# Kernel tuning notes

Measured on AMD Instinct MI355X. Metric: run time of the kernel, lower is better.

The kernel has to match this reference:

```python
import jax, jax.numpy as jnp
import numpy as np

N_OCC, N_SKILL, N_EDGE = 20000, 50000, 600000
D_IN, HID, OUT = 256, 128, 64


def _sage(x_src, x_dst, src, dst, Wl, bl, Wr, n_dst):
    """PyG SAGEConv((in,in),out): mean-aggregate neighbor msgs, lin_l + lin_r(x_dst)."""
    msg = x_src[src]                                        # [E, h] gather
    agg = jax.ops.segment_sum(msg, dst, num_segments=n_dst) # [n_dst, h]
    cnt = jax.ops.segment_sum(jnp.ones((src.shape[0],), x_src.dtype), dst,
                              num_segments=n_dst)
    mean = agg / jnp.maximum(cnt, 1.0)[:, None]
    return mean @ Wl + bl + x_dst @ Wr


def setup_inputs() -> dict:
    key = jax.random.key(0)
    ks = jax.random.split(key, 24)
    f32 = jnp.float32

    def lin(k, fi, fo):
        return jax.random.normal(k, (fi, fo), f32) / np.sqrt(fi)

    inp = {
        "x_occ": jax.random.normal(ks[0], (N_OCC, D_IN), f32),
        "x_skill": jax.random.normal(ks[1], (N_SKILL, D_IN), f32),
        "edge_occ": jax.random.randint(ks[2], (N_EDGE,), 0, N_OCC, jnp.int32),
        "edge_skill": jax.random.randint(ks[3], (N_EDGE,), 0, N_SKILL, jnp.int32),
        # input projections (nn.Linear with bias)
        "pW_occ": lin(ks[4], D_IN, HID), "pb_occ": jnp.zeros((HID,), f32),
        "pW_skill": lin(ks[5], D_IN, HID), "pb_skill": jnp.zeros((HID,), f32),
        # conv1: occ->skill and skill->occ SAGEConvs (lin_l has bias, lin_r none)
        "c1_os_Wl": lin(ks[6], HID, HID), "c1_os_bl": jnp.zeros((HID,), f32),
        "c1_os_Wr": lin(ks[7], HID, HID),
        "c1_so_Wl": lin(ks[8], HID, HID), "c1_so_bl": jnp.zeros((HID,), f32),
        "c1_so_Wr": lin(ks[9], HID, HID),
        # conv2
        "c2_os_Wl": lin(ks[10], HID, OUT), "c2_os_bl": jnp.zeros((OUT,), f32),
        "c2_os_Wr": lin(ks[11], HID, OUT),
        "c2_so_Wl": lin(ks[12], HID, OUT), "c2_so_bl": jnp.zeros((OUT,), f32),
        "c2_so_Wr": lin(ks[13], HID, OUT),
    }
    return inp


def reference(x_occ, x_skill, edge_occ, edge_skill,
              pW_occ, pb_occ, pW_skill, pb_skill,
              c1_os_Wl, c1_os_bl, c1_os_Wr, c1_so_Wl, c1_so_bl, c1_so_Wr,
              c2_os_Wl, c2_os_bl, c2_os_Wr, c2_so_Wl, c2_so_bl, c2_so_Wr):
    n_occ, n_skill = x_occ.shape[0], x_skill.shape[0]
    # input proj + relu
    h_occ = jax.nn.relu(x_occ @ pW_occ + pb_occ)
    h_skill = jax.nn.relu(x_skill @ pW_skill + pb_skill)
    # conv1 (HeteroConv aggr='sum'; each node type receives exactly one conv)
    s1 = _sage(h_occ, h_skill, edge_occ, edge_skill, c1_os_Wl, c1_os_bl, c1_os_Wr, n_skill)
    o1 = _sage(h_skill, h_occ, edge_skill, edge_occ, c1_so_Wl, c1_so_bl, c1_so_Wr, n_occ)
    o1, s1 = jax.nn.relu(o1), jax.nn.relu(s1)
    # conv2
    s2 = _sage(o1, s1, edge_occ, edge_skill, c2_os_Wl, c2_os_bl, c2_os_Wr, n_skill)
    o2 = _sage(s1, o1, edge_skill, edge_occ, c2_so_Wl, c2_so_bl, c2_so_Wr, n_occ)
    return o2, s2
```

## Files before the change

kernel.cpp:

```cpp
#include <hip/hip_runtime.h>

#define N_OCC   20000
#define N_SKILL 50000
#define N_EDGE  600000
#define D_IN    256
#define HID     128
#define OUT_F   64

typedef short bf16x8 __attribute__((ext_vector_type(8)));
typedef float f32x4  __attribute__((ext_vector_type(4)));

__device__ __forceinline__ float bf2f(unsigned short u){
  return __uint_as_float(((unsigned)u) << 16);
}
__device__ __forceinline__ unsigned f2bf_bits(float f){
  unsigned i = __float_as_uint(f);
  return (i + 0x7fffu + ((i >> 16) & 1u)) >> 16;
}
__device__ __forceinline__ unsigned f2bf_bits_u(unsigned i){
  return (i + 0x7fffu + ((i >> 16) & 1u)) >> 16;
}
__device__ __forceinline__ unsigned short f2bf(float f){ return (unsigned short)f2bf_bits(f); }

__device__ __forceinline__ void gload_lds16(const void* g, void* l){
  __builtin_amdgcn_global_load_lds(
      (const __attribute__((address_space(1))) unsigned int*)g,
      (__attribute__((address_space(3))) unsigned int*)l, 16, 0, 0);
}

__global__ void k_detect(const unsigned short* __restrict__ x, int* __restrict__ flag){
  int lane = threadIdx.x & 63;
  int cnt = 0;
  for (int i = lane; i < 1024; i += 64){
    unsigned e = ((unsigned)x[i] >> 7) & 0xFFu;
    if (e >= 0xE0u) cnt++;
  }
  #pragma unroll
  for (int s = 1; s < 64; s <<= 1) cnt += __shfl_xor(cnt, s, 64);
  if (lane == 0) *flag = (cnt >= 8) ? 1 : 0;
}

#define NT_CONV 18
struct ConvTable {
  const void*     src[NT_CONV];
  unsigned short* dst[NT_CONV];
  int             n[NT_CONV];
  int             isx[NT_CONV];
  int             blk_off[NT_CONV + 1];
};

__global__ void k_convert(ConvTable t, const int* __restrict__ flag){
  int isf32 = *flag;
  int b = blockIdx.x;
  int ti = 0;
  while (ti < NT_CONV - 1 && b >= t.blk_off[ti + 1]) ti++;
  if (!isf32 && t.isx[ti]) return;
  int lb = b - t.blk_off[ti];
  int i = (lb * 256 + (int)threadIdx.x) * 8;
  if (i >= t.n[ti]) return;
  unsigned short* dst = t.dst[ti];
  if (isf32){
    const float* s = (const float*)t.src[ti];
    uint4 lo = *(const uint4*)(s + i);
    uint4 hi = *(const uint4*)(s + i + 4);
    uint4 o;
    o.x = f2bf_bits_u(lo.x) | (f2bf_bits_u(lo.y) << 16);
    o.y = f2bf_bits_u(lo.z) | (f2bf_bits_u(lo.w) << 16);
    o.z = f2bf_bits_u(hi.x) | (f2bf_bits_u(hi.y) << 16);
    o.w = f2bf_bits_u(hi.z) | (f2bf_bits_u(hi.w) << 16);
    *(uint4*)(dst + i) = o;
  } else {
    *(uint4*)(dst + i) = *(const uint4*)((const unsigned short*)t.src[ti] + i);
  }
}

__global__ void k_transpose_all(
    const unsigned short* pWo, unsigned short* tWo,
    const unsigned short* pWs, unsigned short* tWs,
    const unsigned short* w2,  unsigned short* t2,
    const unsigned short* w3,  unsigned short* t3,
    const unsigned short* w4,  unsigned short* t4,
    const unsigned short* w5,  unsigned short* t5,
    const unsigned short* w6,  unsigned short* t6,
    const unsigned short* w7,  unsigned short* t7,
    const unsigned short* w8,  unsigned short* t8,
    const unsigned short* w9,  unsigned short* t9)
{
  int idx = blockIdx.x * blockDim.x + threadIdx.x;
  const unsigned short* in; unsigned short* out; int K, N, base;
  if      (idx <  32768){ in=pWo; out=tWo; K=256; N=128; base=0; }
  else if (idx <  65536){ in=pWs; out=tWs; K=256; N=128; base=32768; }
  else if (idx <  81920){ in=w2;  out=t2;  K=128; N=128; base=65536; }
  else if (idx <  98304){ in=w3;  out=t3;  K=128; N=128; base=81920; }
  else if (idx < 114688){ in=w4;  out=t4;  K=128; N=128; base=98304; }
  else if (idx < 131072){ in=w5;  out=t5;  K=128; N=128; base=114688; }
  else if (idx < 139264){ in=w6;  out=t6;  K=128; N=64;  base=131072; }
  else if (idx < 147456){ in=w7;  out=t7;  K=128; N=64;  base=139264; }
  else if (idx < 155648){ in=w8;  out=t8;  K=128; N=64;  base=147456; }
  else if (idx < 163840){ in=w9;  out=t9;  K=128; N=64;  base=155648; }
  else return;
  int li = idx - base;
  int k = li / N, n = li - k * N;
  out[n * K + k] = in[li];
}

#define EPB      4096
#define BIN_BLKS ((N_EDGE + EPB - 1) / EPB)
#define SH_S 9
#define SH_O 8
#define NB_S ((N_SKILL + (1 << SH_S) - 1) >> SH_S)
#define NB_O ((N_OCC   + (1 << SH_O) - 1) >> SH_O)

__launch_bounds__(256)
__global__ void k_bincount(const int* __restrict__ eo, const int* __restrict__ es,
                           int* __restrict__ bkcnt_s, int* __restrict__ bkcnt_o)
{
  int b = blockIdx.x;
  int side = (b >= BIN_BLKS) ? 1 : 0;
  int lb = side ? b - BIN_BLKS : b;
  const int* dste = side ? eo : es;
  int* bkcnt = side ? bkcnt_o : bkcnt_s;
  const int NB = side ? NB_O : NB_S;
  const int SH = side ? SH_O : SH_S;
  __shared__ int cntL[NB_S];
  for (int i = threadIdx.x; i < NB; i += 256) cntL[i] = 0;
  __syncthreads();
  int e0 = lb * EPB, e1 = min(e0 + EPB, N_EDGE);
  for (int e = e0 + threadIdx.x; e < e1; e += 256)
    atomicAdd(&cntL[dste[e] >> SH], 1);
  __syncthreads();
  for (int i = threadIdx.x; i < NB; i += 256)
    if (cntL[i]) atomicAdd(&bkcnt[i], cntL[i]);
}

__global__ void k_bscan(const int* __restrict__ bkcnt_s, const int* __restrict__ bkcnt_o,
                        int* __restrict__ boff_s, int* __restrict__ boff_o,
                        int* __restrict__ off_s, int* __restrict__ off_o)
{
  __shared__ int sc[128];
  int t = threadIdx.x;
  int v = (t < NB_S) ? bkcnt_s[t] : 0;
  sc[t] = v;
  __syncthreads();
  for (int d = 1; d < 128; d <<= 1){
    int u = (t >= d) ? sc[t - d] : 0;
    __syncthreads();
    sc[t] += u;
    __syncthreads();
  }
  if (t < NB_S) boff_s[t] = sc[t] - v;
  if (t == 0){ boff_s[NB_S] = N_EDGE; off_s[N_SKILL] = N_EDGE; }
  __syncthreads();
  int v2 = (t < NB_O) ? bkcnt_o[t] : 0;
  sc[t] = v2;
  __syncthreads();
  for (int d = 1; d < 128; d <<= 1){
    int u = (t >= d) ? sc[t - d] : 0;
    __syncthreads();
    sc[t] += u;
    __syncthreads();
  }
  if (t < NB_O) boff_o[t] = sc[t] - v2;
  if (t == 0){ boff_o[NB_O] = N_EDGE; off_o[N_OCC] = N_EDGE; }
}

__launch_bounds__(256)
__global__ void k_bin(const int* __restrict__ eo, const int* __restrict__ es,
                      const int* __restrict__ boff_s, const int* __restrict__ boff_o,
                      int* __restrict__ bcur_s, int* __restrict__ bcur_o,
                      unsigned* __restrict__ pair_s, unsigned* __restrict__ pair_o)
{
  int b = blockIdx.x;
  int side = (b >= BIN_BLKS) ? 1 : 0;
  int lb = side ? b - BIN_BLKS : b;
  const int* dste = side ? eo : es;
  const int* srce = side ? es : eo;
  const int* boff = side ? boff_o : boff_s;
  int* bcur       = side ? bcur_o : bcur_s;
  unsigned* pairs = side ? pair_o : pair_s;
  const int NB = side ? NB_O : NB_S;
  const int SH = side ? SH_O : SH_S;

  __shared__ int cntL[NB_S], gbaseL[NB_S], lbaseL[NB_S], runL[NB_S];
  __shared__ int sc[128];
  __shared__ unsigned stage[EPB];
  __shared__ int gpos[EPB];

  int e0 = lb * EPB;
  int e1 = min(e0 + EPB, N_EDGE);

  for (int i = threadIdx.x; i < NB; i += 256){ cntL[i] = 0; runL[i] = 0; }
  __syncthreads();
  for (int e = e0 + threadIdx.x; e < e1; e += 256)
    atomicAdd(&cntL[dste[e] >> SH], 1);
  __syncthreads();
  if (threadIdx.x < 128) sc[threadIdx.x] = (threadIdx.x < NB) ? cntL[threadIdx.x] : 0;
  __syncthreads();
  for (int d = 1; d < 128; d <<= 1){
    int v = 0;
    if (threadIdx.x < 128 && threadIdx.x >= d) v = sc[threadIdx.x - d];
    __syncthreads();
    if (threadIdx.x < 128) sc[threadIdx.x] += v;
    __syncthreads();
  }
  if (threadIdx.x < NB){
    int c = cntL[threadIdx.x];
    lbaseL[threadIdx.x] = sc[threadIdx.x] - c;
    gbaseL[threadIdx.x] = boff[threadIdx.x] + atomicAdd(&bcur[threadIdx.x], c);
  }
  __syncthreads();
  for (int e = e0 + threadIdx.x; e < e1; e += 256){
    int d = dste[e], s = srce[e];
    int bk = d >> SH;
    int r = atomicAdd(&runL[bk], 1);
    int lp = lbaseL[bk] + r;
    stage[lp] = ((unsigned)(d & ((1 << SH) - 1)) << 16) | (unsigned)s;
    gpos[lp] = gbaseL[bk] + r;
  }
  __syncthreads();
  int tot = e1 - e0;
  for (int i = threadIdx.x; i < tot; i += 256)
    pairs[gpos[i]] = stage[i];
}

__launch_bounds__(256)
__global__ void k_build(const unsigned* __restrict__ pair_s, const unsigned* __restrict__ pair_o,
                        const int* __restrict__ boff_s, const int* __restrict__ boff_o,
                        int* __restrict__ off_s, int* __restrict__ off_o,
                        int* __restrict__ csr_s, int* __restrict__ csr_o)
{
  int b = blockIdx.x;
  int side = (b >= NB_S) ? 1 : 0;
  int lb = side ? b - NB_S : b;
  const unsigned* pairs = side ? pair_o : pair_s;
  const int* boff = side ? boff_o : boff_s;
  int* off = side ? off_o : off_s;
  int* csr = side ? csr_o : csr_s;
  int SH = side ? SH_O : SH_S;
  int nd_tot = side ? N_OCC : N_SKILL;
  int d0 = lb << SH;
  int d1 = min(d0 + (1 << SH), nd_tot);
  int nd = d1 - d0;
  int p0 = boff[lb], p1 = boff[lb + 1];

  __shared__ int cntL[1 << SH_S];
  __shared__ int offL[1 << SH_S];
  __shared__ int ws[4];
  int t = threadIdx.x;
  cntL[t] = 0; cntL[t + 256] = 0;
  __syncthreads();
  for (int i = p0 + t; i < p1; i += 256)
    atomicAdd(&cntL[pairs[i] >> 16], 1);
  __syncthreads();
  int a0 = cntL[2 * t], a1 = cntL[2 * t + 1];
  int s = a0 + a1;
  int lane = t & 63, wv = t >> 6;
  int x = s;
  #pragma unroll
  for (int d = 1; d < 64; d <<= 1){ int u = __shfl_up(x, d, 64); if (lane >= d) x += u; }
  if (lane == 63) ws[wv] = x;
  __syncthreads();
  int woff = 0;
  for (int w = 0; w < wv; ++w) woff += ws[w];
  int excl = woff + x - s;
  offL[2 * t] = excl;
  offL[2 * t + 1] = excl + a0;
  __syncthreads();
  for (int i = t; i < nd; i += 256) off[d0 + i] = p0 + offL[i];
  cntL[t] = 0; cntL[t + 256] = 0;
  __syncthreads();
  for (int i = p0 + t; i < p1; i += 256){
    unsigned pr = pairs[i];
    int d = (int)(pr >> 16);
    int p = p0 + offL[d] + atomicAdd(&cntL[d], 1);
    csr[p] = (int)(pr & 0xFFFFu);
  }
}

__launch_bounds__(256)
__global__ void k_seg_mean2(const unsigned short* __restrict__ feat0,
                            const int* __restrict__ off0, const int* __restrict__ csr0,
                            unsigned short* __restrict__ out0, int n0, int nb0,
                            const unsigned short* __restrict__ feat1,
                            const int* __restrict__ off1, const int* __restrict__ csr1,
                            unsigned short* __restrict__ out1, int n1)
{
  int b = blockIdx.x;
  int side = (b >= nb0) ? 1 : 0;
  const unsigned short* feat = side ? feat1 : feat0;
  const int* off = side ? off1 : off0;
  const int* csr = side ? csr1 : csr0;
  unsigned short* out = side ? out1 : out0;
  int n_dst = side ? n1 : n0;
  int gw = (side ? b - nb0 : b) * 4 + (int)(threadIdx.x >> 6);
  if (gw >= n_dst) return;
  int lane = threadIdx.x & 63;
  int r = lane >> 4;
  int c = lane & 15;
  int beg = off[gw], end = off[gw + 1];
  float acc[8];
  #pragma unroll
  for (int j = 0; j < 8; ++j) acc[j] = 0.0f;
  for (int e = beg + r; e < end; e += 4){
    int s = csr[e];
    uint4 v = *(const uint4*)(feat + ((size_t)s << 7) + (c << 3));
    acc[0] += __uint_as_float(v.x << 16); acc[1] += __uint_as_float(v.x & 0xffff0000u);
    acc[2] += __uint_as_float(v.y << 16); acc[3] += __uint_as_float(v.y & 0xffff0000u);
    acc[4] += __uint_as_float(v.z << 16); acc[5] += __uint_as_float(v.z & 0xffff0000u);
    acc[6] += __uint_as_float(v.w << 16); acc[7] += __uint_as_float(v.w & 0xffff0000u);
  }
  #pragma unroll
  for (int j = 0; j < 8; ++j){
    acc[j] += __shfl_xor(acc[j], 16, 64);
    acc[j] += __shfl_xor(acc[j], 32, 64);
  }
  if (r == 0){
    int cnt = end - beg;
    float inv = 1.0f / (float)(cnt > 0 ? cnt : 1);
    uint4 o;
    o.x = f2bf_bits(acc[0] * inv) | (f2bf_bits(acc[1] * inv) << 16);
    o.y = f2bf_bits(acc[2] * inv) | (f2bf_bits(acc[3] * inv) << 16);
    o.z = f2bf_bits(acc[4] * inv) | (f2bf_bits(acc[5] * inv) << 16);
    o.w = f2bf_bits(acc[6] * inv) | (f2bf_bits(acc[7] * inv) << 16);
    *(uint4*)(out + ((size_t)gw << 7) + (c << 3)) = o;
  }
}

__launch_bounds__(256)
__global__ void k_seg_out2(const unsigned short* __restrict__ Pg0, const unsigned short* __restrict__ Ps0,
                           const int* __restrict__ off0, const int* __restrict__ csr0,
                           const unsigned short* __restrict__ bias0, size_t o_off0, int n0, int nb0,
                           const unsigned short* __restrict__ Pg1, const unsigned short* __restrict__ Ps1,
                           const int* __restrict__ off1, const int* __restrict__ csr1,
                           const unsigned short* __restrict__ bias1, size_t o_off1, int n1,
                           void* __restrict__ out, const int* __restrict__ wire_flag)
{
  int b = blockIdx.x;
  int side = (b >= nb0) ? 1 : 0;
  const unsigned short* Pg = side ? Pg1 : Pg0;
  const unsigned short* Ps = side ? Ps1 : Ps0;
  const int* off = side ? off1 : off0;
  const int* csr = side ? csr1 : csr0;
  const unsigned short* bias = side ? bias1 : bias0;
  size_t o_off = side ? o_off1 : o_off0;
  int n_dst = side ? n1 : n0;
  int gw = (side ? b - nb0 : b) * 4 + (int)(threadIdx.x >> 6);
  if (gw >= n_dst) return;
  int lane = threadIdx.x & 63;
  int r = lane >> 3;
  int c = lane & 7;
  int beg = off[gw], end = off[gw + 1];
  float acc[8];
  #pragma unroll
  for (int j = 0; j < 8; ++j) acc[j] = 0.0f;
  for (int e = beg + r; e < end; e += 8){
    int s = csr[e];
    uint4 v = *(const uint4*)(Pg + ((size_t)s << 7) + (c << 3));
    acc[0] += __uint_as_float(v.x << 16); acc[1] += __uint_as_float(v.x & 0xffff0000u);
    acc[2] += __uint_as_float(v.y << 16); acc[3] += __uint_as_float(v.y & 0xffff0000u);
    acc[4] += __uint_as_float(v.z << 16); acc[5] += __uint_as_float(v.z & 0xffff0000u);
    acc[6] += __uint_as_float(v.w << 16); acc[7] += __uint_as_float(v.w & 0xffff0000u);
  }
  #pragma unroll
  for (int j = 0; j < 8; ++j){
    acc[j] += __shfl_xor(acc[j], 8, 64);
    acc[j] += __shfl_xor(acc[j], 16, 64);
    acc[j] += __shfl_xor(acc[j], 32, 64);
  }
  if (r == 0){
    int cnt = end - beg;
    float inv = 1.0f / (float)(cnt > 0 ? cnt : 1);
    uint4 sv = *(const uint4*)(Ps + ((size_t)gw << 7) + 64 + (c << 3));
    uint4 bv = *(const uint4*)(bias + (c << 3));
    float o0 = acc[0] * inv + __uint_as_float(sv.x << 16)         + __uint_as_float(bv.x << 16);
    float o1 = acc[1] * inv + __uint_as_float(sv.x & 0xffff0000u) + __uint_as_float(bv.x & 0xffff0000u);
    float o2 = acc[2] * inv + __uint_as_float(sv.y << 16)         + __uint_as_float(bv.y << 16);
    float o3 = acc[3] * inv + __uint_as_float(sv.y & 0xffff0000u) + __uint_as_float(bv.y & 0xffff0000u);
    float o4 = acc[4] * inv + __uint_as_float(sv.z << 16)         + __uint_as_float(bv.z << 16);
    float o5 = acc[5] * inv + __uint_as_float(sv.z & 0xffff0000u) + __uint_as_float(bv.z & 0xffff0000u);
    float o6 = acc[6] * inv + __uint_as_float(sv.w << 16)         + __uint_as_float(bv.w << 16);
    float o7 = acc[7] * inv + __uint_as_float(sv.w & 0xffff0000u) + __uint_as_float(bv.w & 0xffff0000u);
    size_t eoff = o_off + (size_t)gw * 64 + (c << 3);
    if (*wire_flag){
      float* op = (float*)out + eoff;
      uint4 w0, w1;
      w0.x = __float_as_uint(o0); w0.y = __float_as_uint(o1);
      w0.z = __float_as_uint(o2); w0.w = __float_as_uint(o3);
      w1.x = __float_as_uint(o4); w1.y = __float_as_uint(o5);
      w1.z = __float_as_uint(o6); w1.w = __float_as_uint(o7);
      *(uint4*)op = w0;
      *(uint4*)(op + 4) = w1;
    } else {
      unsigned short* op = (unsigned short*)out + eoff;
      uint4 w;
      w.x = f2bf_bits(o0) | (f2bf_bits(o1) << 16);
      w.y = f2bf_bits(o2) | (f2bf_bits(o3) << 16);
      w.z = f2bf_bits(o4) | (f2bf_bits(o5) << 16);
      w.w = f2bf_bits(o6) | (f2bf_bits(o7) << 16);
      *(uint4*)op = w;
    }
  }
}

template<int K1, int HASA2, int AW>
__launch_bounds__(256)
__global__ void k_gemm4(const unsigned short* __restrict__ A1a_0, const unsigned short* __restrict__ A1a_1,
                        const unsigned short* __restrict__ A1b_0, const unsigned short* __restrict__ A1b_1,
                        const unsigned short* __restrict__ W1T_0, const unsigned short* __restrict__ W1T_1,
                        const unsigned short* __restrict__ A2_0, const unsigned short* __restrict__ A2_1,
                        const unsigned short* __restrict__ W2T_0, const unsigned short* __restrict__ W2T_1,
                        const unsigned short* __restrict__ bias_0, const unsigned short* __restrict__ bias_1,
                        unsigned short* __restrict__ C_0, unsigned short* __restrict__ C_1,
                        int nb0, int do_relu, const int* __restrict__ wire_flag)
{
  constexpr int TM    = 80;
  constexpr int ROWB  = K1 * 2;
  constexpr int TILEB = TM * ROWB;
  constexpr int ITERS = TILEB / 4096;
  constexpr int NK    = K1 / 32;
  constexpr int RSH   = (K1 == 256) ? 9 : 8;

  __shared__ unsigned short lds[(HASA2 ? 2 : 1) * TM * K1];

  int b = blockIdx.x;
  int side = (b >= nb0) ? 1 : 0;
  int lb = side ? b - nb0 : b;
  const unsigned short* A1a = side ? A1a_1 : A1a_0;
  const unsigned short* A1b = side ? A1b_1 : A1b_0;
  const unsigned short* W1T = side ? W1T_1 : W1T_0;
  const unsigned short* A2  = side ? A2_1  : A2_0;
  const unsigned short* W2T = side ? W2T_1 : W2T_0;
  const unsigned short* bias= side ? bias_1: bias_0;
  unsigned short* C = side ? C_1 : C_0;

  const unsigned short* A1 = (AW && *wire_flag) ? A1b : A1a;
  const int tid = threadIdx.x;

  {
    const char* a1base = (const char*)A1 + (size_t)lb * TILEB;
    #pragma unroll
    for (int it = 0; it < ITERS; ++it){
      int L = (it * 256 + tid) * 16;
      int row = L >> RSH;
      int cb  = L & (ROWB - 1);
      int gb  = row * ROWB + (cb ^ ((row & 7) << 4));
      gload_lds16(a1base + gb, (char*)lds + L);
    }
    if (HASA2){
      const char* a2base = (const char*)A2 + (size_t)lb * TILEB;
      #pragma unroll
      for (int it = 0; it < ITERS; ++it){
        int L = (it * 256 + tid) * 16;
        int row = L >> RSH;
        int cb  = L & (ROWB - 1);
        int gb  = row * ROWB + (cb ^ ((row & 7) << 4));
        gload_lds16(a2base + gb, (char*)lds + TILEB + L);
      }
    }
  }

  const int lane = tid & 63;
  const int wv   = tid >> 6;
  const int q    = lane >> 4;
  const int mr   = lane & 15;
  const int koff = q * 8;

  bf16x8 b1[2][NK];
  #pragma unroll
  for (int nt = 0; nt < 2; ++nt){
    const unsigned short* bp = W1T + (size_t)(wv * 32 + nt * 16 + mr) * K1 + koff;
    #pragma unroll
    for (int k = 0; k < NK; ++k)
      b1[nt][k] = *(const bf16x8*)(bp + k * 32);
  }
  bf16x8 b2[2][HASA2 ? NK : 1];
  if (HASA2){
    #pragma unroll
    for (int nt = 0; nt < 2; ++nt){
      const unsigned short* bp = W2T + (size_t)(wv * 32 + nt * 16 + mr) * K1 + koff;
      #pragma unroll
      for (int k = 0; k < NK; ++k)
        b2[nt][k] = *(const bf16x8*)(bp + k * 32);
    }
  }

  __syncthreads();

  f32x4 acc[5][2];
  #pragma unroll
  for (int rt = 0; rt < 5; ++rt)
    #pragma unroll
    for (int nt = 0; nt < 2; ++nt)
      #pragma unroll
      for (int j = 0; j < 4; ++j) acc[rt][nt][j] = 0.0f;

  #pragma unroll
  for (int rt = 0; rt < 5; ++rt){
    const int rl = rt * 16 + mr;
    const int sw = (rl & 7) << 4;
    #pragma unroll
    for (int k = 0; k < NK; ++k){
      const int cb = k * 64 + q * 16;
      bf16x8 a = *(const bf16x8*)((const char*)lds + rl * ROWB + (cb ^ sw));
      #pragma unroll
      for (int nt = 0; nt < 2; ++nt)
        acc[rt][nt] = __builtin_amdgcn_mfma_f32_16x16x32_bf16(a, b1[nt][k], acc[rt][nt], 0, 0, 0);
      if (HASA2){
        bf16x8 a2 = *(const bf16x8*)((const char*)lds + TILEB + rl * ROWB + (cb ^ sw));
        #pragma unroll
        for (int nt = 0; nt < 2; ++nt)
          acc[rt][nt] = __builtin_amdgcn_mfma_f32_16x16x32_bf16(a2, b2[nt][k], acc[rt][nt], 0, 0, 0);
      }
    }
  }

  #pragma unroll
  for (int rt = 0; rt < 5; ++rt){
    #pragma unroll
    for (int nt = 0; nt < 2; ++nt){
      int col = wv * 32 + nt * 16 + mr;
      float bv = bf2f(bias[col]);
      #pragma unroll
      for (int r4 = 0; r4 < 4; ++r4){
        int orow = lb * TM + rt * 16 + q * 4 + r4;
        float v = acc[rt][nt][r4] + bv;
        if (do_relu) v = fmaxf(v, 0.0f);
        C[(size_t)orow * 128 + col] = f2bf(v);
      }
    }
  }
}

extern "C" void kernel_launch(void* const* d_in, const int* in_sizes, int n_in,
                              void* d_out, int out_size, void* d_ws, size_t ws_size,
                              hipStream_t stream)
{
  const void* raw[20];
  for (int i = 0; i < 20; ++i) raw[i] = d_in[i];
  const int* edge_occ   = (const int*)d_in[2];
  const int* edge_skill = (const int*)d_in[3];

  char* ws = (char*)d_ws;
  size_t off = 0;
  auto alloc = [&](size_t bytes) -> char* {
    char* p = ws + off;
    off = (off + bytes + 255) & ~(size_t)255;
    return p;
  };

  int* wire_flag = (int*)alloc(4);

  static const int cn[NT_CONV] = {
    N_OCC * D_IN, N_SKILL * D_IN,
    D_IN * HID, HID, D_IN * HID, HID,
    HID * HID, HID, HID * HID,
    HID * HID, HID, HID * HID,
    HID * OUT_F, OUT_F, HID * OUT_F,
    HID * OUT_F, OUT_F, HID * OUT_F
  };
  static const int raw_idx[NT_CONV] = {0,1, 4,5,6,7, 8,9,10, 11,12,13, 14,15,16, 17,18,19};
  static const int isx[NT_CONV]     = {1,1, 0,0,0,0, 0,0,0,  0,0,0,    0,0,0,    0,0,0};
  unsigned short* can[NT_CONV];
  for (int i = 0; i < NT_CONV; ++i) can[i] = (unsigned short*)alloc((size_t)cn[i] * 2);

  ConvTable ct;
  ct.blk_off[0] = 0;
  for (int i = 0; i < NT_CONV; ++i){
    ct.src[i] = raw[raw_idx[i]];
    ct.dst[i] = can[i];
    ct.n[i]   = cn[i];
    ct.isx[i] = isx[i];
    ct.blk_off[i + 1] = ct.blk_off[i] + (cn[i] + 2047) / 2048;
  }
  const int conv_blocks = ct.blk_off[NT_CONV];

  const unsigned short* can_xocc = can[0], *can_xskl = can[1];
  const unsigned short* c_pWo = can[2],  *c_pbo = can[3];
  const unsigned short* c_pWs = can[4],  *c_pbs = can[5];
  const unsigned short* c1osWl = can[6], *c1osbl = can[7], *c1osWr = can[8];
  const unsigned short* c1soWl = can[9], *c1sobl = can[10], *c1soWr = can[11];
  const unsigned short* c2osWl = can[12], *c2osbl = can[13], *c2osWr = can[14];
  const unsigned short* c2soWl = can[15], *c2sobl = can[16], *c2soWr = can[17];

  unsigned short* wt_pocc   = (unsigned short*)alloc(32768 * 2);
  unsigned short* wt_pskill = (unsigned short*)alloc(32768 * 2);
  unsigned short* wt_c1osWl = (unsigned short*)alloc(16384 * 2);
  unsigned short* wt_c1osWr = (unsigned short*)alloc(16384 * 2);
  unsigned short* wt_c1soWl = (unsigned short*)alloc(16384 * 2);
  unsigned short* wt_c1soWr = (unsigned short*)alloc(16384 * 2);
  unsigned short* comb_occ  = (unsigned short*)alloc(16384 * 2);
  unsigned short* comb_skl  = (unsigned short*)alloc(16384 * 2);

  size_t zero_bytes = (size_t)(2 * (NB_S + NB_O)) * 4 + 256;
  char* zero_base = alloc(zero_bytes);
  int* bkcnt_s = (int*)zero_base;
  int* bkcnt_o = bkcnt_s + NB_S;
  int* bcur_s  = bkcnt_o + NB_O;
  int* bcur_o  = bcur_s + NB_S;
  unsigned short* zbias = (unsigned short*)(bcur_o + NB_O);

  int* boff_s = (int*)alloc((NB_S + 1) * 4);
  int* boff_o = (int*)alloc((NB_O + 1) * 4);
  int* off_s = (int*)alloc((N_SKILL + 1) * 4);
  int* off_o = (int*)alloc((N_OCC + 1) * 4);
  int* csr_s = (int*)alloc((size_t)N_EDGE * 4);
  int* csr_o = (int*)alloc((size_t)N_EDGE * 4);
  unsigned* pair_s = (unsigned*)alloc((size_t)N_EDGE * 4);
  unsigned* pair_o = (unsigned*)alloc((size_t)N_EDGE * 4);

  unsigned short* h_occ   = (unsigned short*)alloc((size_t)N_OCC * HID * 2);
  unsigned short* h_skill = (unsigned short*)alloc((size_t)N_SKILL * HID * 2);
  unsigned short* mean_s  = (unsigned short*)alloc((size_t)N_SKILL * HID * 2);
  unsigned short* mean_o  = (unsigned short*)alloc((size_t)N_OCC * HID * 2);
  unsigned short* s1      = (unsigned short*)alloc((size_t)N_SKILL * HID * 2);
  unsigned short* o1      = (unsigned short*)alloc((size_t)N_OCC * HID * 2);
  unsigned short* P_occ   = (unsigned short*)alloc((size_t)N_OCC * HID * 2);
  unsigned short* P_skl   = (unsigned short*)alloc((size_t)N_SKILL * HID * 2);

  const int GT_OCC = N_OCC / 80;
  const int GT_SKL = N_SKILL / 80;
  const int SM_SKL = (N_SKILL + 3) / 4;
  const int SM_OCC = (N_OCC + 3) / 4;

  hipMemsetAsync(zero_base, 0, zero_bytes, stream);

  k_detect<<<1, 64, 0, stream>>>((const unsigned short*)raw[0], wire_flag);
  k_convert<<<conv_blocks, 256, 0, stream>>>(ct, wire_flag);

  k_transpose_all<<<640, 256, 0, stream>>>(
      c_pWo, wt_pocc, c_pWs, wt_pskill,
      c1osWl, wt_c1osWl, c1osWr, wt_c1osWr,
      c1soWl, wt_c1soWl, c1soWr, wt_c1soWr,
      c2osWl, comb_occ,
      c2osWr, comb_skl + 64 * 128,
      c2soWl, comb_skl,
      c2soWr, comb_occ + 64 * 128);

  k_bincount<<<2 * BIN_BLKS, 256, 0, stream>>>(edge_occ, edge_skill, bkcnt_s, bkcnt_o);
  k_bscan<<<1, 128, 0, stream>>>(bkcnt_s, bkcnt_o, boff_s, boff_o, off_s, off_o);
  k_bin<<<2 * BIN_BLKS, 256, 0, stream>>>(edge_occ, edge_skill, boff_s, boff_o,
                                          bcur_s, bcur_o, pair_s, pair_o);
  k_build<<<NB_S + NB_O, 256, 0, stream>>>(pair_s, pair_o, boff_s, boff_o,
                                           off_s, off_o, csr_s, csr_o);

  k_gemm4<256, 0, 1><<<GT_OCC + GT_SKL, 256, 0, stream>>>(
      (const unsigned short*)raw[0], (const unsigned short*)raw[1],
      can_xocc, can_xskl,
      wt_pocc, wt_pskill, nullptr, nullptr, nullptr, nullptr,
      c_pbo, c_pbs, h_occ, h_skill, GT_OCC, 1, wire_flag);

  k_seg_mean2<<<SM_SKL + SM_OCC, 256, 0, stream>>>(
      h_occ, off_s, csr_s, mean_s, N_SKILL, SM_SKL,
      h_skill, off_o, csr_o, mean_o, N_OCC);

  k_gemm4<128, 1, 0><<<GT_SKL + GT_OCC, 256, 0, stream>>>(
      mean_s, mean_o, mean_s, mean_o,
      wt_c1osWl, wt_c1soWl,
      h_skill, h_occ, wt_c1osWr, wt_c1soWr,
      c1osbl, c1sobl, s1, o1, GT_SKL, 1, wire_flag);

  k_gemm4<128, 0, 0><<<GT_OCC + GT_SKL, 256, 0, stream>>>(
      o1, s1, o1, s1,
      comb_occ, comb_skl, nullptr, nullptr, nullptr, nullptr,
      zbias, zbias, P_occ, P_skl, GT_OCC, 0, wire_flag);

  k_seg_out2<<<SM_SKL + SM_OCC, 256, 0, stream>>>(
      P_occ, P_skl, off_s, csr_s, c2osbl, (size_t)N_OCC * OUT_F, N_SKILL, SM_SKL,
      P_skl, P_occ, off_o, csr_o, c2sobl, 0, N_OCC,
      d_out, wire_flag);
}
```

Before: 322.4 us.

## Gather from column-chunked feature layout and fold dtype detection into convert

The GEMMs now also write their outputs in a column-chunked layout: 16-column slices for the projection output and 8-column slices for the conv2 projection. The segment-mean and segment-output kernels are relaunched so that each block handles one feature chunk for 32 destination nodes. The goal is to keep each chunk's gathered source rows small enough to stay in cache and to improve locality of the random gathers. The separate detect kernel is removed, and every convert block now recomputes the fp32/bf16 probe itself. This adds extra strided stores in the GEMM epilogue and duplicate gathers of the CSR indices across the 8 chunks.

```diff
diff --git a/kernel.cpp b/kernel.cpp
--- a/kernel.cpp
+++ b/kernel.cpp
@@ -26,18 +26,6 @@
   __builtin_amdgcn_global_load_lds(
       (const __attribute__((address_space(1))) unsigned int*)g,
       (__attribute__((address_space(3))) unsigned int*)l, 16, 0, 0);
-}
-
-__global__ void k_detect(const unsigned short* __restrict__ x, int* __restrict__ flag){
-  int lane = threadIdx.x & 63;
-  int cnt = 0;
-  for (int i = lane; i < 1024; i += 64){
-    unsigned e = ((unsigned)x[i] >> 7) & 0xFFu;
-    if (e >= 0xE0u) cnt++;
-  }
-  #pragma unroll
-  for (int s = 1; s < 64; s <<= 1) cnt += __shfl_xor(cnt, s, 64);
-  if (lane == 0) *flag = (cnt >= 8) ? 1 : 0;
 }
 
 #define NT_CONV 18
@@ -49,14 +37,28 @@
   int             blk_off[NT_CONV + 1];
 };
 
-__global__ void k_convert(ConvTable t, const int* __restrict__ flag){
-  int isf32 = *flag;
+__global__ void k_convert(ConvTable t, const unsigned short* __restrict__ xprobe,
+                          int* __restrict__ flag){
+  __shared__ int wsum[4];
+  int tid = threadIdx.x;
+  int cnt = 0;
+  for (int i = tid; i < 1024; i += 256){
+    unsigned e = ((unsigned)xprobe[i] >> 7) & 0xFFu;
+    if (e >= 0xE0u) cnt++;
+  }
+  #pragma unroll
+  for (int s = 1; s < 64; s <<= 1) cnt += __shfl_xor(cnt, s, 64);
+  if ((tid & 63) == 0) wsum[tid >> 6] = cnt;
+  __syncthreads();
+  int isf32 = (wsum[0] + wsum[1] + wsum[2] + wsum[3]) >= 8;
+  if (blockIdx.x == 0 && tid == 0) *flag = isf32;
+
   int b = blockIdx.x;
   int ti = 0;
   while (ti < NT_CONV - 1 && b >= t.blk_off[ti + 1]) ti++;
   if (!isf32 && t.isx[ti]) return;
   int lb = b - t.blk_off[ti];
-  int i = (lb * 256 + (int)threadIdx.x) * 8;
+  int i = (lb * 256 + tid) * 8;
   if (i >= t.n[ti]) return;
   unsigned short* dst = t.dst[ti];
   if (isf32){
@@ -278,32 +280,40 @@
 }
 
 __launch_bounds__(256)
-__global__ void k_seg_mean2(const unsigned short* __restrict__ feat0,
+__global__ void k_seg_mean3(const unsigned short* __restrict__ fcm0,
                             const int* __restrict__ off0, const int* __restrict__ csr0,
-                            unsigned short* __restrict__ out0, int n0, int nb0,
-                            const unsigned short* __restrict__ feat1,
+                            unsigned short* __restrict__ out0, int n0, int ns0, int nbb0,
+                            const unsigned short* __restrict__ fcm1,
                             const int* __restrict__ off1, const int* __restrict__ csr1,
-                            unsigned short* __restrict__ out1, int n1)
+                            unsigned short* __restrict__ out1, int n1, int ns1)
 {
   int b = blockIdx.x;
-  int side = (b >= nb0) ? 1 : 0;
-  const unsigned short* feat = side ? feat1 : feat0;
+  int side = (b >= nbb0) ? 1 : 0;
+  int lb = side ? b - nbb0 : b;
+  const unsigned short* fcm = side ? fcm1 : fcm0;
   const int* off = side ? off1 : off0;
   const int* csr = side ? csr1 : csr0;
   unsigned short* out = side ? out1 : out0;
   int n_dst = side ? n1 : n0;
-  int gw = (side ? b - nb0 : b) * 4 + (int)(threadIdx.x >> 6);
+  int nsrc  = side ? ns1 : ns0;
+  int fc = lb & 7;
+  int g  = lb >> 3;
+  int tid = threadIdx.x;
+  int lane = tid & 63;
+  int wv = tid >> 6;
+  int d8 = lane >> 3;
+  int s  = (lane >> 1) & 3;
+  int c  = lane & 1;
+  int gw = g * 32 + wv * 8 + d8;
   if (gw >= n_dst) return;
-  int lane = threadIdx.x & 63;
-  int r = lane >> 4;
-  int c = lane & 15;
+  const unsigned short* slice = fcm + (size_t)fc * nsrc * 16 + c * 8;
   int beg = off[gw], end = off[gw + 1];
   float acc[8];
   #pragma unroll
   for (int j = 0; j < 8; ++j) acc[j] = 0.0f;
-  for (int e = beg + r; e < end; e += 4){
-    int s = csr[e];
-    uint4 v = *(const uint4*)(feat + ((size_t)s << 7) + (c << 3));
+  for (int e = beg + s; e < end; e += 4){
+    int si = csr[e];
+    uint4 v = *(const uint4*)(slice + (size_t)si * 16);
     acc[0] += __uint_as_float(v.x << 16); acc[1] += __uint_as_float(v.x & 0xffff0000u);
     acc[2] += __uint_as_float(v.y << 16); acc[3] += __uint_as_float(v.y & 0xffff0000u);
     acc[4] += __uint_as_float(v.z << 16); acc[5] += __uint_as_float(v.z & 0xffff0000u);
@@ -311,10 +321,10 @@
   }
   #pragma unroll
   for (int j = 0; j < 8; ++j){
-    acc[j] += __shfl_xor(acc[j], 16, 64);
-    acc[j] += __shfl_xor(acc[j], 32, 64);
-  }
-  if (r == 0){
+    acc[j] += __shfl_xor(acc[j], 2, 64);
+    acc[j] += __shfl_xor(acc[j], 4, 64);
+  }
+  if (s == 0){
     int cnt = end - beg;
     float inv = 1.0f / (float)(cnt > 0 ? cnt : 1);
     uint4 o;
@@ -322,21 +332,24 @@
     o.y = f2bf_bits(acc[2] * inv) | (f2bf_bits(acc[3] * inv) << 16);
     o.z = f2bf_bits(acc[4] * inv) | (f2bf_bits(acc[5] * inv) << 16);
     o.w = f2bf_bits(acc[6] * inv) | (f2bf_bits(acc[7] * inv) << 16);
-    *(uint4*)(out + ((size_t)gw << 7) + (c << 3)) = o;
+    *(uint4*)(out + (size_t)gw * 128 + fc * 16 + c * 8) = o;
   }
 }
 
 __launch_bounds__(256)
-__global__ void k_seg_out2(const unsigned short* __restrict__ Pg0, const unsigned short* __restrict__ Ps0,
+__global__ void k_seg_out3(const unsigned short* __restrict__ Pg0, const unsigned short* __restrict__ Ps0,
                            const int* __restrict__ off0, const int* __restrict__ csr0,
-                           const unsigned short* __restrict__ bias0, size_t o_off0, int n0, int nb0,
+                           const unsigned short* __restrict__ bias0, size_t o_off0,
+                           int n0, int ns0, int nbb0,
                            const unsigned short* __restrict__ Pg1, const unsigned short* __restrict__ Ps1,
                            const int* __restrict__ off1, const int* __restrict__ csr1,
-                           const unsigned short* __restrict__ bias1, size_t o_off1, int n1,
+                           const unsigned short* __restrict__ bias1, size_t o_off1,
+                           int n1, int ns1,
                            void* __restrict__ out, const int* __restrict__ wire_flag)
 {
   int b = blockIdx.x;
-  int side = (b >= nb0) ? 1 : 0;
+  int side = (b >= nbb0) ? 1 : 0;
+  int lb = side ? b - nbb0 : b;
   const unsigned short* Pg = side ? Pg1 : Pg0;
   const unsigned short* Ps = side ? Ps1 : Ps0;
   const int* off = side ? off1 : off0;
@@ -344,18 +357,24 @@
   const unsigned short* bias = side ? bias1 : bias0;
   size_t o_off = side ? o_off1 : o_off0;
   int n_dst = side ? n1 : n0;
-  int gw = (side ? b - nb0 : b) * 4 + (int)(threadIdx.x >> 6);
+  int nsrc  = side ? ns1 : ns0;
+  int fc = lb & 7;
+  int g  = lb >> 3;
+  int tid = threadIdx.x;
+  int lane = tid & 63;
+  int wv = tid >> 6;
+  int d8 = lane >> 3;
+  int s  = lane & 7;
+  int gw = g * 32 + wv * 8 + d8;
   if (gw >= n_dst) return;
-  int lane = threadIdx.x & 63;
-  int r = lane >> 3;
-  int c = lane & 7;
+  const unsigned short* gsl = Pg + (size_t)fc * nsrc * 8;
   int beg = off[gw], end = off[gw + 1];
   float acc[8];
   #pragma unroll
   for (int j = 0; j < 8; ++j) acc[j] = 0.0f;
-  for (int e = beg + r; e < end; e += 8){
-    int s = csr[e];
-    uint4 v = *(const uint4*)(Pg + ((size_t)s << 7) + (c << 3));
+  for (int e = beg + s; e < end; e += 8){
+    int si = csr[e];
+    uint4 v = *(const uint4*)(gsl + (size_t)si * 8);
     acc[0] += __uint_as_float(v.x << 16); acc[1] += __uint_as_float(v.x & 0xffff0000u);
     acc[2] += __uint_as_float(v.y << 16); acc[3] += __uint_as_float(v.y & 0xffff0000u);
     acc[4] += __uint_as_float(v.z << 16); acc[5] += __uint_as_float(v.z & 0xffff0000u);
@@ -363,15 +382,15 @@
   }
   #pragma unroll
   for (int j = 0; j < 8; ++j){
-    acc[j] += __shfl_xor(acc[j], 8, 64);
-    acc[j] += __shfl_xor(acc[j], 16, 64);
-    acc[j] += __shfl_xor(acc[j], 32, 64);
-  }
-  if (r == 0){
+    acc[j] += __shfl_xor(acc[j], 1, 64);
+    acc[j] += __shfl_xor(acc[j], 2, 64);
+    acc[j] += __shfl_xor(acc[j], 4, 64);
+  }
+  if (s == 0){
     int cnt = end - beg;
     float inv = 1.0f / (float)(cnt > 0 ? cnt : 1);
-    uint4 sv = *(const uint4*)(Ps + ((size_t)gw << 7) + 64 + (c << 3));
-    uint4 bv = *(const uint4*)(bias + (c << 3));
+    uint4 sv = *(const uint4*)(Ps + (size_t)(8 + fc) * n_dst * 8 + (size_t)gw * 8);
+    uint4 bv = *(const uint4*)(bias + fc * 8);
     float o0 = acc[0] * inv + __uint_as_float(sv.x << 16)         + __uint_as_float(bv.x << 16);
     float o1 = acc[1] * inv + __uint_as_float(sv.x & 0xffff0000u) + __uint_as_float(bv.x & 0xffff0000u);
     float o2 = acc[2] * inv + __uint_as_float(sv.y << 16)         + __uint_as_float(bv.y << 16);
@@ -380,7 +399,7 @@
     float o5 = acc[5] * inv + __uint_as_float(sv.z & 0xffff0000u) + __uint_as_float(bv.z & 0xffff0000u);
     float o6 = acc[6] * inv + __uint_as_float(sv.w << 16)         + __uint_as_float(bv.w << 16);
     float o7 = acc[7] * inv + __uint_as_float(sv.w & 0xffff0000u) + __uint_as_float(bv.w & 0xffff0000u);
-    size_t eoff = o_off + (size_t)gw * 64 + (c << 3);
+    size_t eoff = o_off + (size_t)gw * 64 + fc * 8;
     if (*wire_flag){
       float* op = (float*)out + eoff;
       uint4 w0, w1;
@@ -402,7 +421,7 @@
   }
 }
 
-template<int K1, int HASA2, int AW>
+template<int K1, int HASA2, int AW, int CMODE>
 __launch_bounds__(256)
 __global__ void k_gemm4(const unsigned short* __restrict__ A1a_0, const unsigned short* __restrict__ A1a_1,
                         const unsigned short* __restrict__ A1b_0, const unsigned short* __restrict__ A1b_1,
@@ -411,6 +430,8 @@
                         const unsigned short* __restrict__ W2T_0, const unsigned short* __restrict__ W2T_1,
                         const unsigned short* __restrict__ bias_0, const unsigned short* __restrict__ bias_1,
                         unsigned short* __restrict__ C_0, unsigned short* __restrict__ C_1,
+                        unsigned short* __restrict__ CM_0, unsigned short* __restrict__ CM_1,
+                        int ncm0, int ncm1,
                         int nb0, int do_relu, const int* __restrict__ wire_flag)
 {
   constexpr int TM    = 80;
@@ -431,7 +452,9 @@
   const unsigned short* A2  = side ? A2_1  : A2_0;
   const unsigned short* W2T = side ? W2T_1 : W2T_0;
   const unsigned short* bias= side ? bias_1: bias_0;
-  unsigned short* C = side ? C_1 : C_0;
+  unsigned short* C  = side ? C_1  : C_0;
+  unsigned short* CM = side ? CM_1 : CM_0;
+  const size_t ncm = (size_t)(side ? ncm1 : ncm0);
 
   const unsigned short* A1 = (AW && *wire_flag) ? A1b : A1a;
   const int tid = threadIdx.x;
@@ -525,7 +548,12 @@
         int orow = lb * TM + rt * 16 + q * 4 + r4;
         float v = acc[rt][nt][r4] + bv;
         if (do_relu) v = fmaxf(v, 0.0f);
-        C[(size_t)orow * 128 + col] = f2bf(v);
+        unsigned short bits = f2bf(v);
+        if constexpr (CMODE != 2) C[(size_t)orow * 128 + col] = bits;
+        if constexpr (CMODE == 1)
+          CM[((size_t)(col >> 4) * ncm + orow) * 16 + (col & 15)] = bits;
+        if constexpr (CMODE == 2)
+          CM[((size_t)(col >> 3) * ncm + orow) * 8 + (col & 7)] = bits;
       }
     }
   }
@@ -608,24 +636,25 @@
   unsigned* pair_s = (unsigned*)alloc((size_t)N_EDGE * 4);
   unsigned* pair_o = (unsigned*)alloc((size_t)N_EDGE * 4);
 
-  unsigned short* h_occ   = (unsigned short*)alloc((size_t)N_OCC * HID * 2);
-  unsigned short* h_skill = (unsigned short*)alloc((size_t)N_SKILL * HID * 2);
-  unsigned short* mean_s  = (unsigned short*)alloc((size_t)N_SKILL * HID * 2);
-  unsigned short* mean_o  = (unsigned short*)alloc((size_t)N_OCC * HID * 2);
-  unsigned short* s1      = (unsigned short*)alloc((size_t)N_SKILL * HID * 2);
-  unsigned short* o1      = (unsigned short*)alloc((size_t)N_OCC * HID * 2);
-  unsigned short* P_occ   = (unsigned short*)alloc((size_t)N_OCC * HID * 2);
-  unsigned short* P_skl   = (unsigned short*)alloc((size_t)N_SKILL * HID * 2);
+  unsigned short* h_occ    = (unsigned short*)alloc((size_t)N_OCC * HID * 2);
+  unsigned short* h_skill  = (unsigned short*)alloc((size_t)N_SKILL * HID * 2);
+  unsigned short* hcm_occ  = (unsigned short*)alloc((size_t)N_OCC * HID * 2);
+  unsigned short* hcm_skl  = (unsigned short*)alloc((size_t)N_SKILL * HID * 2);
+  unsigned short* mean_s   = (unsigned short*)alloc((size_t)N_SKILL * HID * 2);
+  unsigned short* mean_o   = (unsigned short*)alloc((size_t)N_OCC * HID * 2);
+  unsigned short* s1       = (unsigned short*)alloc((size_t)N_SKILL * HID * 2);
+  unsigned short* o1       = (unsigned short*)alloc((size_t)N_OCC * HID * 2);
+  unsigned short* Pcm_occ  = (unsigned short*)alloc((size_t)N_OCC * HID * 2);
+  unsigned short* Pcm_skl  = (unsigned short*)alloc((size_t)N_SKILL * HID * 2);
 
   const int GT_OCC = N_OCC / 80;
   const int GT_SKL = N_SKILL / 80;
-  const int SM_SKL = (N_SKILL + 3) / 4;
-  const int SM_OCC = (N_OCC + 3) / 4;
+  const int SG_SKL = 8 * ((N_SKILL + 31) / 32);
+  const int SG_OCC = 8 * ((N_OCC + 31) / 32);
 
   hipMemsetAsync(zero_base, 0, zero_bytes, stream);
 
-  k_detect<<<1, 64, 0, stream>>>((const unsigned short*)raw[0], wire_flag);
-  k_convert<<<conv_blocks, 256, 0, stream>>>(ct, wire_flag);
+  k_convert<<<conv_blocks, 256, 0, stream>>>(ct, (const unsigned short*)raw[0], wire_flag);
 
   k_transpose_all<<<640, 256, 0, stream>>>(
       c_pWo, wt_pocc, c_pWs, wt_pskill,
@@ -643,29 +672,32 @@
   k_build<<<NB_S + NB_O, 256, 0, stream>>>(pair_s, pair_o, boff_s, boff_o,
                                            off_s, off_o, csr_s, csr_o);
 
-  k_gemm4<256, 0, 1><<<GT_OCC + GT_SKL, 256, 0, stream>>>(
+  k_gemm4<256, 0, 1, 1><<<GT_OCC + GT_SKL, 256, 0, stream>>>(
       (const unsigned short*)raw[0], (const unsigned short*)raw[1],
       can_xocc, can_xskl,
       wt_pocc, wt_pskill, nullptr, nullptr, nullptr, nullptr,
-      c_pbo, c_pbs, h_occ, h_skill, GT_OCC, 1, wire_flag);
-
-  k_seg_mean2<<<SM_SKL + SM_OCC, 256, 0, stream>>>(
-      h_occ, off_s, csr_s, mean_s, N_SKILL, SM_SKL,
-      h_skill, off_o, csr_o, mean_o, N_OCC);
-
-  k_gemm4<128, 1, 0><<<GT_SKL + GT_OCC, 256, 0, stream>>>(
+      c_pbo, c_pbs, h_occ, h_skill, hcm_occ, hcm_skl, N_OCC, N_SKILL,
+      GT_OCC, 1, wire_flag);
+
+  k_seg_mean3<<<SG_SKL + SG_OCC, 256, 0, stream>>>(
+      hcm_occ, off_s, csr_s, mean_s, N_SKILL, N_OCC, SG_SKL,
+      hcm_skl, off_o, csr_o, mean_o, N_OCC, N_SKILL);
+
+  k_gemm4<128, 1, 0, 0><<<GT_SKL + GT_OCC, 256, 0, stream>>>(
       mean_s, mean_o, mean_s, mean_o,
       wt_c1osWl, wt_c1soWl,
       h_skill, h_occ, wt_c1osWr, wt_c1soWr,
-      c1osbl, c1sobl, s1, o1, GT_SKL, 1, wire_flag);
-
-  k_gemm4<128, 0, 0><<<GT_OCC + GT_SKL, 256, 0, stream>>>(
+      c1osbl, c1sobl, s1, o1, nullptr, nullptr, 0, 0,
+      GT_SKL, 1, wire_flag);
+
+  k_gemm4<128, 0, 0, 2><<<GT_OCC + GT_SKL, 256, 0, stream>>>(
       o1, s1, o1, s1,
       comb_occ, comb_skl, nullptr, nullptr, nullptr, nullptr,
-      zbias, zbias, P_occ, P_skl, GT_OCC, 0, wire_flag);
-
-  k_seg_out2<<<SM_SKL + SM_OCC, 256, 0, stream>>>(
-      P_occ, P_skl, off_s, csr_s, c2osbl, (size_t)N_OCC * OUT_F, N_SKILL, SM_SKL,
-      P_skl, P_occ, off_o, csr_o, c2sobl, 0, N_OCC,
+      zbias, zbias, Pcm_occ, Pcm_skl, Pcm_occ, Pcm_skl, N_OCC, N_SKILL,
+      GT_OCC, 0, wire_flag);
+
+  k_seg_out3<<<SG_SKL + SG_OCC, 256, 0, stream>>>(
+      Pcm_occ, Pcm_skl, off_s, csr_s, c2osbl, (size_t)N_OCC * OUT_F, N_SKILL, N_OCC, SG_SKL,
+      Pcm_skl, Pcm_occ, off_o, csr_o, c2sobl, 0, N_OCC, N_SKILL,
       d_out, wire_flag);
 }
```

New measurement: 366.7 us. 13.8% more time.
